# Optimization experiments

Hardware: AMD Instinct MI355X
Metric: run time of the kernel (lower is better)

## Reference

```python
import jax, jax.numpy as jnp
import numpy as np

B, TQ, TK, D, H = 8, 1024, 1024, 1024, 16
HD = D // H
EPS = 1e-5


def layernorm(x, g, b):
    mu = jnp.mean(x, axis=-1, keepdims=True)
    var = jnp.mean(jnp.square(x - mu), axis=-1, keepdims=True)
    return (x - mu) * jax.lax.rsqrt(var + EPS) * g + b


def setup_inputs() -> dict:
    key = jax.random.key(0)
    ks = jax.random.split(key, 16)
    s = 1.0 / np.sqrt(D)
    return {
        "base": jax.random.normal(ks[0], (B, TQ, D), jnp.float32),
        "fusion": jax.random.normal(ks[1], (B, TK, D), jnp.float32),
        "Wq": jax.random.normal(ks[2], (D, D), jnp.float32) * s,
        "Wk": jax.random.normal(ks[3], (D, D), jnp.float32) * s,
        "Wv": jax.random.normal(ks[4], (D, D), jnp.float32) * s,
        "Wo": jax.random.normal(ks[5], (D, D), jnp.float32) * s,
        "g1": jnp.ones((D,), jnp.float32),
        "b1": jnp.zeros((D,), jnp.float32),
        "g2": jnp.ones((D,), jnp.float32),
        "b2": jnp.zeros((D,), jnp.float32),
        "fc1_w": jax.random.normal(ks[6], (D, D), jnp.float32) * s,
        "fc1_b": jnp.zeros((D,), jnp.float32),
        "fc2_w": jax.random.normal(ks[7], (D, D), jnp.float32) * s,
        "fc2_b": jnp.zeros((D,), jnp.float32),
        "rw": jax.random.normal(ks[8], (D, D), jnp.float32) * s,
        "rb": jnp.zeros((D,), jnp.float32),
        "alpha": jnp.asarray(0.1, jnp.float32),
    }


def reference(base, fusion, Wq, Wk, Wv, Wo, g1, b1, g2, b2,
              fc1_w, fc1_b, fc2_w, fc2_b, rw, rb, alpha):
    def split_heads(x):  # [B,T,D] -> [B,H,T,hd]
        return x.reshape(B, -1, H, HD).transpose(0, 2, 1, 3)

    Q = split_heads(base @ Wq.T)
    K = split_heads(fusion @ Wk.T)
    V = split_heads(fusion @ Wv.T)

    scores = jnp.einsum("bhqd,bhkd->bhqk", Q, K) / jnp.sqrt(jnp.float32(HD))
    attn = jax.nn.softmax(scores, axis=-1)
    # threshold mask (the torch scatter_ with arange indices is an identity copy)
    masked = attn * (attn >= alpha).astype(attn.dtype)
    # second softmax over masked weights (zeros contribute exp(0)=1, as in the original)
    attn2 = jax.nn.softmax(masked, axis=-1)
    out = jnp.einsum("bhqk,bhkd->bhqd", attn2, V)
    out = out.transpose(0, 2, 1, 3).reshape(B, TQ, D)
    out = out @ Wo.T
    x = layernorm(base + out, g1, b1)  # dropout is eval-mode identity
    ff = jax.nn.silu(jax.nn.silu(x @ fc1_w.T + fc1_b) @ fc2_w.T + fc2_b)
    y = layernorm(x + ff, g2, b2)
    final = y @ rw.T + rb
    return final, masked
```

## Files before the change

kernel.cpp:

```cpp
#include <hip/hip_runtime.h>


typedef unsigned short u16;
typedef __attribute__((ext_vector_type(8))) short  bf16x8;
typedef __attribute__((ext_vector_type(4))) float  f32x4;

#define GLL16(gp, lp) __builtin_amdgcn_global_load_lds(                     \
    (__attribute__((address_space(1))) const void*)(gp),                    \
    (__attribute__((address_space(3))) void*)(lp), 16, 0, 0)

__device__ __forceinline__ u16 f2bf(float x) {
  union { float f; unsigned u; } v; v.f = x;
  return (u16)((v.u + 0x7FFF + ((v.u >> 16) & 1)) >> 16);
}
__device__ __forceinline__ f32x4 zero4() { f32x4 z = {0.f, 0.f, 0.f, 0.f}; return z; }

__global__ __launch_bounds__(256) void pack_act(const float* __restrict__ a,
                                                const float* __restrict__ b,
                                                u16* __restrict__ outa,
                                                u16* __restrict__ outb) {
  size_t i = (size_t)blockIdx.x * 256 + threadIdx.x;
  const float* in = blockIdx.y ? b : a;
  u16* out = blockIdx.y ? outb : outa;
  out[i] = f2bf(in[i]);
}

__global__ __launch_bounds__(256) void pack_w(
    const float* __restrict__ w0, const float* __restrict__ w1,
    const float* __restrict__ w2, const float* __restrict__ w3,
    const float* __restrict__ w4, const float* __restrict__ w5,
    const float* __restrict__ w6, u16* __restrict__ out) {
  size_t i = (size_t)blockIdx.x * 256 + threadIdx.x;
  const float* in;
  switch (blockIdx.y) {
    case 0: in = w0; break;  case 1: in = w1; break;
    case 2: in = w2; break;  case 3: in = w3; break;
    case 4: in = w4; break;  case 5: in = w5; break;
    default: in = w6; break;
  }
  out[(size_t)blockIdx.y * 1048576 + i] = f2bf(in[i]);
}

#define EPI_QKV       0
#define EPI_F32       3
#define EPI_SILU_BF16 4
#define EPI_SILU_F32  5
#define EPI_BIAS_F32  6

template <int EPI>
__global__ __launch_bounds__(256) void gemm_bt(
    const u16* __restrict__ A, int lda,
    const u16* __restrict__ W, int ldw,
    int M, int N, int K,
    float* __restrict__ outF, u16* __restrict__ outU,
    const float* __restrict__ bias,
    const u16* __restrict__ A2) {
  __shared__ u16 As[128 * 32];
  __shared__ u16 Bs[128 * 32];
  int tid = threadIdx.x;
  int l = tid & 63, w = tid >> 6;
  int wr = w >> 1, wc = w & 1, lr = l & 15, lq = l >> 4;
  int m0 = blockIdx.y * 128, n0 = blockIdx.x * 128;

  const u16* Ap = A;
  const u16* Wp = W;
  u16* outUp = outU;
  if constexpr (EPI == EPI_QKV) {
    int z = blockIdx.z;
    if (z) Ap = A2;
    Wp = W + (size_t)z * 1048576;
    outUp = outU + (size_t)z * 8388608;
  }

  f32x4 acc[4][4];
#pragma unroll
  for (int i = 0; i < 4; i++)
#pragma unroll
    for (int j = 0; j < 4; j++) acc[i][j] = zero4();

  auto stage = [&](const u16* src, int ld, int r0, int k0, u16* lds) {
#pragma unroll
    for (int j = 0; j < 2; ++j) {
      int seg = j * 256 + tid;
      int row = seg >> 2, sp = seg & 3;
      const u16* g = src + (size_t)(r0 + row) * ld + k0 +
                     ((sp ^ ((row >> 1) & 3)) << 3);
      GLL16(g, lds + seg * 8);
    }
  };

  int nk = K >> 5;
  stage(Ap, lda, m0, 0, As);
  stage(Wp, ldw, n0, 0, Bs);
  for (int kt = 0; kt < nk; ++kt) {
    __syncthreads();
    bf16x8 af[4], bw[4];
    int slot = (lq ^ ((lr >> 1) & 3)) << 3;
#pragma unroll
    for (int mi = 0; mi < 4; mi++)
      af[mi] = *(const bf16x8*)&As[(wr * 64 + mi * 16 + lr) * 32 + slot];
#pragma unroll
    for (int ni = 0; ni < 4; ni++)
      bw[ni] = *(const bf16x8*)&Bs[(wc * 64 + ni * 16 + lr) * 32 + slot];
#pragma unroll
    for (int mi = 0; mi < 4; mi++)
#pragma unroll
      for (int ni = 0; ni < 4; ni++)
        acc[mi][ni] = __builtin_amdgcn_mfma_f32_16x16x32_bf16(af[mi], bw[ni],
                                                              acc[mi][ni], 0, 0, 0);
    __syncthreads();
    if (kt + 1 < nk) {
      stage(Ap, lda, m0, (kt + 1) << 5, As);
      stage(Wp, ldw, n0, (kt + 1) << 5, Bs);
    }
  }

#pragma unroll
  for (int mi = 0; mi < 4; mi++) {
#pragma unroll
    for (int ni = 0; ni < 4; ni++) {
      int col = n0 + wc * 64 + ni * 16 + lr;
#pragma unroll
      for (int r = 0; r < 4; r++) {
        int row = m0 + wr * 64 + mi * 16 + lq * 4 + r;
        float v = acc[mi][ni][r];
        if constexpr (EPI == EPI_QKV) {
          int b = row >> 10, t = row & 1023, h = col >> 6, d = col & 63;
          int z = blockIdx.z;
          if (z == 0) {
            outUp[((size_t)(b * 16 + h) * 1024 + t) * 64 + d] = f2bf(v);
          } else if (z == 1) {
            size_t base = ((size_t)(b * 16 + h) * 1024 + t) * 64;
            outUp[base + (((d >> 3) ^ (t & 7)) << 3) + (d & 7)] = f2bf(v);
          } else {
            size_t o = ((size_t)(b * 16 + h) * 64 + d) * 1024 + (t & ~63) +
                       ((((t >> 3) & 7) ^ (d & 7)) << 3) + (t & 7);
            outUp[o] = f2bf(v);
          }
        } else if constexpr (EPI == EPI_F32) {
          outF[(size_t)row * N + col] = v;
        } else if constexpr (EPI == EPI_SILU_BF16) {
          float z = v + bias[col];
          outUp[(size_t)row * N + col] = f2bf(z / (1.f + __expf(-z)));
        } else if constexpr (EPI == EPI_SILU_F32) {
          float z = v + bias[col];
          outF[(size_t)row * N + col] = z / (1.f + __expf(-z));
        } else {
          outF[(size_t)row * N + col] = v + bias[col];
        }
      }
    }
  }
}

__global__ __launch_bounds__(256) void attn_kernel(
    const u16* __restrict__ Q2, const u16* __restrict__ K2,
    const u16* __restrict__ Vt, const float* __restrict__ alphap,
    float* __restrict__ masked_out, u16* __restrict__ attn_out) {
  __shared__ __align__(16) u16 Ks[64 * 64];
  __shared__ __align__(16) u16 Vs[64 * 64];
  __shared__ __align__(16) u16 Ps[4][2][16 * 72];

  int tid = threadIdx.x;
  int l = tid & 63, w = tid >> 6, lr = l & 15, lq = l >> 4;
  int q0 = blockIdx.x * 128;
  int h = blockIdx.y, b = blockIdx.z;
  int bh = b * 16 + h;
  const u16* Qb = Q2 + (size_t)bh * 1024 * 64;
  const u16* Kb = K2 + (size_t)bh * 1024 * 64;
  const u16* Vb = Vt + (size_t)bh * 64 * 1024;
  float alpha = alphap[0];
  int qw = q0 + w * 32;

  bf16x8 qf[2][2];
#pragma unroll
  for (int s = 0; s < 2; s++)
#pragma unroll
    for (int kt = 0; kt < 2; kt++)
      qf[s][kt] = *(const bf16x8*)(Qb + (size_t)(qw + s * 16 + lr) * 64 + kt * 32 + lq * 8);

  float s1[2][4] = {{0.f, 0.f, 0.f, 0.f}, {0.f, 0.f, 0.f, 0.f}};

  for (int kc = 0; kc < 16; ++kc) {
    __syncthreads();
#pragma unroll
    for (int j = 0; j < 2; ++j) {
      int seg = j * 256 + tid;
      GLL16(Kb + (size_t)kc * 4096 + seg * 8, Ks + seg * 8);
    }
    __syncthreads();
    f32x4 acc[2][4];
#pragma unroll
    for (int s = 0; s < 2; s++)
#pragma unroll
      for (int ni = 0; ni < 4; ni++) acc[s][ni] = zero4();
#pragma unroll
    for (int ni = 0; ni < 4; ++ni) {
      int t = ni * 16 + lr;
      bf16x8 k0 = *(const bf16x8*)&Ks[t * 64 + (((0 + lq) ^ (lr & 7)) << 3)];
      bf16x8 k1 = *(const bf16x8*)&Ks[t * 64 + (((4 + lq) ^ (lr & 7)) << 3)];
#pragma unroll
      for (int s = 0; s < 2; s++) {
        acc[s][ni] = __builtin_amdgcn_mfma_f32_16x16x32_bf16(qf[s][0], k0, acc[s][ni], 0, 0, 0);
        acc[s][ni] = __builtin_amdgcn_mfma_f32_16x16x32_bf16(qf[s][1], k1, acc[s][ni], 0, 0, 0);
      }
    }
#pragma unroll
    for (int s = 0; s < 2; s++)
#pragma unroll
      for (int ni = 0; ni < 4; ni++)
#pragma unroll
        for (int r = 0; r < 4; r++)
          s1[s][r] += __expf(acc[s][ni][r] * 0.125f);
  }
#pragma unroll
  for (int s = 0; s < 2; s++)
#pragma unroll
    for (int r = 0; r < 4; r++) {
      float v = s1[s][r];
      v += __shfl_xor(v, 1); v += __shfl_xor(v, 2);
      v += __shfl_xor(v, 4); v += __shfl_xor(v, 8);
      s1[s][r] = 1.0f / v;
    }

  float s2[2][4] = {{0.f, 0.f, 0.f, 0.f}, {0.f, 0.f, 0.f, 0.f}};
  f32x4 oacc[2][4];
#pragma unroll
  for (int s = 0; s < 2; s++)
#pragma unroll
    for (int dg = 0; dg < 4; dg++) oacc[s][dg] = zero4();

  for (int kc = 0; kc < 16; ++kc) {
    __syncthreads();
#pragma unroll
    for (int j = 0; j < 2; ++j) {
      int seg = j * 256 + tid;
      GLL16(Kb + (size_t)kc * 4096 + seg * 8, Ks + seg * 8);
    }
#pragma unroll
    for (int j = 0; j < 2; ++j) {
      int seg = j * 256 + tid;
      GLL16(Vb + (size_t)(seg >> 3) * 1024 + kc * 64 + (seg & 7) * 8, Vs + seg * 8);
    }
    __syncthreads();

    f32x4 acc[2][4];
#pragma unroll
    for (int s = 0; s < 2; s++)
#pragma unroll
      for (int ni = 0; ni < 4; ni++) acc[s][ni] = zero4();
#pragma unroll
    for (int ni = 0; ni < 4; ++ni) {
      int t = ni * 16 + lr;
      bf16x8 k0 = *(const bf16x8*)&Ks[t * 64 + (((0 + lq) ^ (lr & 7)) << 3)];
      bf16x8 k1 = *(const bf16x8*)&Ks[t * 64 + (((4 + lq) ^ (lr & 7)) << 3)];
#pragma unroll
      for (int s = 0; s < 2; s++) {
        acc[s][ni] = __builtin_amdgcn_mfma_f32_16x16x32_bf16(qf[s][0], k0, acc[s][ni], 0, 0, 0);
        acc[s][ni] = __builtin_amdgcn_mfma_f32_16x16x32_bf16(qf[s][1], k1, acc[s][ni], 0, 0, 0);
      }
    }

#pragma unroll
    for (int s = 0; s < 2; s++) {
#pragma unroll
      for (int ni = 0; ni < 4; ni++) {
#pragma unroll
        for (int r = 0; r < 4; r++) {
          float e = __expf(acc[s][ni][r] * 0.125f);
          float a = e * s1[s][r];
          a = (a >= alpha) ? a : 0.0f;
          size_t row = (size_t)bh * 1024 + qw + s * 16 + lq * 4 + r;
          masked_out[row * 1024 + kc * 64 + ni * 16 + lr] = a;
          float p = __expf(a);
          s2[s][r] += p;
          Ps[w][s][(lq * 4 + r) * 72 + ni * 16 + lr] = f2bf(p);
        }
      }
    }
    __syncthreads();

    bf16x8 pf[2][2];
#pragma unroll
    for (int s = 0; s < 2; s++)
#pragma unroll
      for (int kt = 0; kt < 2; kt++)
        pf[s][kt] = *(const bf16x8*)&Ps[w][s][lr * 72 + kt * 32 + lq * 8];
#pragma unroll
    for (int dg = 0; dg < 4; dg++) {
      int d = dg * 16 + lr;
      bf16x8 v0 = *(const bf16x8*)&Vs[d * 64 + (((0 + lq) ^ (lr & 7)) << 3)];
      bf16x8 v1 = *(const bf16x8*)&Vs[d * 64 + (((4 + lq) ^ (lr & 7)) << 3)];
#pragma unroll
      for (int s = 0; s < 2; s++) {
        oacc[s][dg] = __builtin_amdgcn_mfma_f32_16x16x32_bf16(pf[s][0], v0, oacc[s][dg], 0, 0, 0);
        oacc[s][dg] = __builtin_amdgcn_mfma_f32_16x16x32_bf16(pf[s][1], v1, oacc[s][dg], 0, 0, 0);
      }
    }
  }

#pragma unroll
  for (int s = 0; s < 2; s++)
#pragma unroll
    for (int r = 0; r < 4; r++) {
      float v = s2[s][r];
      v += __shfl_xor(v, 1); v += __shfl_xor(v, 2);
      v += __shfl_xor(v, 4); v += __shfl_xor(v, 8);
      s2[s][r] = 1.0f / v;
    }
#pragma unroll
  for (int s = 0; s < 2; s++)
#pragma unroll
    for (int dg = 0; dg < 4; dg++)
#pragma unroll
      for (int r = 0; r < 4; r++) {
        int q = qw + s * 16 + lq * 4 + r;
        attn_out[(size_t)(b * 1024 + q) * 1024 + h * 64 + dg * 16 + lr] =
            f2bf(oacc[s][dg][r] * s2[s][r]);
      }
}

__global__ __launch_bounds__(256) void ln_kernel(
    const float* __restrict__ A, const float* __restrict__ Bv,
    const float* __restrict__ g, const float* __restrict__ beta,
    float* __restrict__ outF, u16* __restrict__ outB) {
  __shared__ float red[4];
  int row = blockIdx.x, t = threadIdx.x;
  const float* pa = A + (size_t)row * 1024;
  const float* pb = Bv + (size_t)row * 1024;
  float v[4];
  float s = 0.f;
#pragma unroll
  for (int i = 0; i < 4; i++) { int c = t + 256 * i; v[i] = pa[c] + pb[c]; s += v[i]; }
#pragma unroll
  for (int off = 1; off < 64; off <<= 1) s += __shfl_xor(s, off);
  if ((t & 63) == 0) red[t >> 6] = s;
  __syncthreads();
  s = red[0] + red[1] + red[2] + red[3];
  float mu = s * 0.0009765625f;
  float q = 0.f;
#pragma unroll
  for (int i = 0; i < 4; i++) { float d = v[i] - mu; q += d * d; }
  __syncthreads();
#pragma unroll
  for (int off = 1; off < 64; off <<= 1) q += __shfl_xor(q, off);
  if ((t & 63) == 0) red[t >> 6] = q;
  __syncthreads();
  q = red[0] + red[1] + red[2] + red[3];
  float rs = rsqrtf(q * 0.0009765625f + 1e-5f);
#pragma unroll
  for (int i = 0; i < 4; i++) {
    int c = t + 256 * i;
    float y = (v[i] - mu) * rs * g[c] + beta[c];
    if (outF) outF[(size_t)row * 1024 + c] = y;
    if (outB) outB[(size_t)row * 1024 + c] = f2bf(y);
  }
}

#define WS_BASEB   0
#define WS_FUSB    16777216
#define WS_W       33554432
#define WS_QKV     48234496
#define WS_ATTNO   98566144
#define WS_O       115343360
#define WS_X       148897792
#define WS_XB      WS_BASEB
#define WS_H1      WS_ATTNO
#define WS_FF      WS_QKV
#define WS_YB      (WS_QKV + 33554432)

extern "C" void kernel_launch(void* const* d_in, const int* in_sizes, int n_in,
                              void* d_out, int out_size, void* d_ws, size_t ws_size,
                              hipStream_t stream) {
  const float* base   = (const float*)d_in[0];
  const float* fusion = (const float*)d_in[1];
  const float* Wq     = (const float*)d_in[2];
  const float* Wk     = (const float*)d_in[3];
  const float* Wv     = (const float*)d_in[4];
  const float* Wo     = (const float*)d_in[5];
  const float* g1     = (const float*)d_in[6];
  const float* b1     = (const float*)d_in[7];
  const float* g2     = (const float*)d_in[8];
  const float* b2     = (const float*)d_in[9];
  const float* fc1w   = (const float*)d_in[10];
  const float* fc1b   = (const float*)d_in[11];
  const float* fc2w   = (const float*)d_in[12];
  const float* fc2b   = (const float*)d_in[13];
  const float* rw     = (const float*)d_in[14];
  const float* rb     = (const float*)d_in[15];
  const float* alphap = (const float*)d_in[16];

  char* ws = (char*)d_ws;
  u16* baseb  = (u16*)(ws + WS_BASEB);
  u16* fusb   = (u16*)(ws + WS_FUSB);
  u16* wall   = (u16*)(ws + WS_W);
  u16* Q2     = (u16*)(ws + WS_QKV);
  u16* attno  = (u16*)(ws + WS_ATTNO);
  float* obuf = (float*)(ws + WS_O);
  float* x    = (float*)(ws + WS_X);
  u16* xb     = (u16*)(ws + WS_XB);
  u16* h1     = (u16*)(ws + WS_H1);
  float* ff   = (float*)(ws + WS_FF);
  u16* yb     = (u16*)(ws + WS_YB);

  float* final_out  = (float*)d_out;
  float* masked_out = final_out + 8388608;

  pack_act<<<dim3(32768, 2), 256, 0, stream>>>(base, fusion, baseb, fusb);
  pack_w<<<dim3(4096, 7), 256, 0, stream>>>(Wq, Wk, Wv, Wo, fc1w, fc2w, rw, wall);

  dim3 gg(8, 64);

  gemm_bt<EPI_QKV><<<dim3(8, 64, 3), 256, 0, stream>>>(
      baseb, 1024, wall, 1024, 8192, 1024, 1024, nullptr, Q2, nullptr, fusb);

  attn_kernel<<<dim3(8, 16, 8), 256, 0, stream>>>(
      Q2, Q2 + 8388608, Q2 + 16777216, alphap, masked_out, attno);

  gemm_bt<EPI_F32><<<gg, 256, 0, stream>>>(attno, 1024, wall + 3 * 1048576, 1024,
                                           8192, 1024, 1024, obuf, nullptr, nullptr, nullptr);
  ln_kernel<<<8192, 256, 0, stream>>>(base, obuf, g1, b1, x, xb);

  gemm_bt<EPI_SILU_BF16><<<gg, 256, 0, stream>>>(xb, 1024, wall + 4 * 1048576, 1024,
                                                 8192, 1024, 1024, nullptr, h1, fc1b, nullptr);
  gemm_bt<EPI_SILU_F32><<<gg, 256, 0, stream>>>(h1, 1024, wall + 5 * 1048576, 1024,
                                                8192, 1024, 1024, ff, nullptr, fc2b, nullptr);
  ln_kernel<<<8192, 256, 0, stream>>>(x, ff, g2, b2, nullptr, yb);

  gemm_bt<EPI_BIAS_F32><<<gg, 256, 0, stream>>>(yb, 1024, wall + 6 * 1048576, 1024,
                                                8192, 1024, 1024, final_out, nullptr, rb, nullptr);
}
```

Baseline: 1.054 ms.

## Double-buffer LDS tiles in GEMM and attention; store intermediates as bf16

The GEMM and both attention passes now use ping-pong LDS buffers. The next K/V or A/W tile is issued with global_load_lds before the current tile is computed, which removes one barrier per iteration. The Wo and fc2 GEMM outputs are written as bf16 instead of fp32, and the layernorm kernel reads them as bf16, halving intermediate traffic at some precision cost. In the attention PV stage a barrier is replaced by an lgkmcnt wait. With one barrier per iteration, the async global-to-LDS loads into the other buffer may not be fenced correctly, which risks a race.

```diff
diff --git a/kernel.cpp b/kernel.cpp
--- a/kernel.cpp
+++ b/kernel.cpp
@@ -12,6 +12,10 @@
 __device__ __forceinline__ u16 f2bf(float x) {
   union { float f; unsigned u; } v; v.f = x;
   return (u16)((v.u + 0x7FFF + ((v.u >> 16) & 1)) >> 16);
+}
+__device__ __forceinline__ float bf2f(u16 h) {
+  union { unsigned u; float f; } v; v.u = ((unsigned)h) << 16;
+  return v.f;
 }
 __device__ __forceinline__ f32x4 zero4() { f32x4 z = {0.f, 0.f, 0.f, 0.f}; return z; }
 
@@ -42,9 +46,8 @@
 }
 
 #define EPI_QKV       0
-#define EPI_F32       3
+#define EPI_BF16      1
 #define EPI_SILU_BF16 4
-#define EPI_SILU_F32  5
 #define EPI_BIAS_F32  6
 
 template <int EPI>
@@ -55,8 +58,8 @@
     float* __restrict__ outF, u16* __restrict__ outU,
     const float* __restrict__ bias,
     const u16* __restrict__ A2) {
-  __shared__ u16 As[128 * 32];
-  __shared__ u16 Bs[128 * 32];
+  __shared__ u16 As[2][128 * 32];
+  __shared__ u16 Bs[2][128 * 32];
   int tid = threadIdx.x;
   int l = tid & 63, w = tid >> 6;
   int wr = w >> 1, wc = w & 1, lr = l & 15, lq = l >> 4;
@@ -90,29 +93,30 @@
   };
 
   int nk = K >> 5;
-  stage(Ap, lda, m0, 0, As);
-  stage(Wp, ldw, n0, 0, Bs);
+  stage(Ap, lda, m0, 0, As[0]);
+  stage(Wp, ldw, n0, 0, Bs[0]);
   for (int kt = 0; kt < nk; ++kt) {
     __syncthreads();
+    if (kt + 1 < nk) {
+      stage(Ap, lda, m0, (kt + 1) << 5, As[(kt + 1) & 1]);
+      stage(Wp, ldw, n0, (kt + 1) << 5, Bs[(kt + 1) & 1]);
+    }
+    const u16* Ab = As[kt & 1];
+    const u16* Bb = Bs[kt & 1];
     bf16x8 af[4], bw[4];
     int slot = (lq ^ ((lr >> 1) & 3)) << 3;
 #pragma unroll
     for (int mi = 0; mi < 4; mi++)
-      af[mi] = *(const bf16x8*)&As[(wr * 64 + mi * 16 + lr) * 32 + slot];
+      af[mi] = *(const bf16x8*)&Ab[(wr * 64 + mi * 16 + lr) * 32 + slot];
 #pragma unroll
     for (int ni = 0; ni < 4; ni++)
-      bw[ni] = *(const bf16x8*)&Bs[(wc * 64 + ni * 16 + lr) * 32 + slot];
+      bw[ni] = *(const bf16x8*)&Bb[(wc * 64 + ni * 16 + lr) * 32 + slot];
 #pragma unroll
     for (int mi = 0; mi < 4; mi++)
 #pragma unroll
       for (int ni = 0; ni < 4; ni++)
         acc[mi][ni] = __builtin_amdgcn_mfma_f32_16x16x32_bf16(af[mi], bw[ni],
                                                               acc[mi][ni], 0, 0, 0);
-    __syncthreads();
-    if (kt + 1 < nk) {
-      stage(Ap, lda, m0, (kt + 1) << 5, As);
-      stage(Wp, ldw, n0, (kt + 1) << 5, Bs);
-    }
   }
 
 #pragma unroll
@@ -137,14 +141,11 @@
                        ((((t >> 3) & 7) ^ (d & 7)) << 3) + (t & 7);
             outUp[o] = f2bf(v);
           }
-        } else if constexpr (EPI == EPI_F32) {
-          outF[(size_t)row * N + col] = v;
+        } else if constexpr (EPI == EPI_BF16) {
+          outUp[(size_t)row * N + col] = f2bf(v);
         } else if constexpr (EPI == EPI_SILU_BF16) {
           float z = v + bias[col];
           outUp[(size_t)row * N + col] = f2bf(z / (1.f + __expf(-z)));
-        } else if constexpr (EPI == EPI_SILU_F32) {
-          float z = v + bias[col];
-          outF[(size_t)row * N + col] = z / (1.f + __expf(-z));
         } else {
           outF[(size_t)row * N + col] = v + bias[col];
         }
@@ -157,8 +158,8 @@
     const u16* __restrict__ Q2, const u16* __restrict__ K2,
     const u16* __restrict__ Vt, const float* __restrict__ alphap,
     float* __restrict__ masked_out, u16* __restrict__ attn_out) {
-  __shared__ __align__(16) u16 Ks[64 * 64];
-  __shared__ __align__(16) u16 Vs[64 * 64];
+  __shared__ __align__(16) u16 Ks[2][4096];
+  __shared__ __align__(16) u16 Vs[2][4096];
   __shared__ __align__(16) u16 Ps[4][2][16 * 72];
 
   int tid = threadIdx.x;
@@ -172,6 +173,21 @@
   float alpha = alphap[0];
   int qw = q0 + w * 32;
 
+  auto stageK = [&](int kc, u16* dst) {
+#pragma unroll
+    for (int j = 0; j < 2; ++j) {
+      int seg = j * 256 + tid;
+      GLL16(Kb + (size_t)kc * 4096 + seg * 8, dst + seg * 8);
+    }
+  };
+  auto stageV = [&](int kc, u16* dst) {
+#pragma unroll
+    for (int j = 0; j < 2; ++j) {
+      int seg = j * 256 + tid;
+      GLL16(Vb + (size_t)(seg >> 3) * 1024 + kc * 64 + (seg & 7) * 8, dst + seg * 8);
+    }
+  };
+
   bf16x8 qf[2][2];
 #pragma unroll
   for (int s = 0; s < 2; s++)
@@ -181,14 +197,11 @@
 
   float s1[2][4] = {{0.f, 0.f, 0.f, 0.f}, {0.f, 0.f, 0.f, 0.f}};
 
+  stageK(0, Ks[0]);
   for (int kc = 0; kc < 16; ++kc) {
     __syncthreads();
-#pragma unroll
-    for (int j = 0; j < 2; ++j) {
-      int seg = j * 256 + tid;
-      GLL16(Kb + (size_t)kc * 4096 + seg * 8, Ks + seg * 8);
-    }
-    __syncthreads();
+    if (kc + 1 < 16) stageK(kc + 1, Ks[(kc + 1) & 1]);
+    const u16* Kc = Ks[kc & 1];
     f32x4 acc[2][4];
 #pragma unroll
     for (int s = 0; s < 2; s++)
@@ -197,8 +210,8 @@
 #pragma unroll
     for (int ni = 0; ni < 4; ++ni) {
       int t = ni * 16 + lr;
-      bf16x8 k0 = *(const bf16x8*)&Ks[t * 64 + (((0 + lq) ^ (lr & 7)) << 3)];
-      bf16x8 k1 = *(const bf16x8*)&Ks[t * 64 + (((4 + lq) ^ (lr & 7)) << 3)];
+      bf16x8 k0 = *(const bf16x8*)&Kc[t * 64 + (((0 + lq) ^ (lr & 7)) << 3)];
+      bf16x8 k1 = *(const bf16x8*)&Kc[t * 64 + (((4 + lq) ^ (lr & 7)) << 3)];
 #pragma unroll
       for (int s = 0; s < 2; s++) {
         acc[s][ni] = __builtin_amdgcn_mfma_f32_16x16x32_bf16(qf[s][0], k0, acc[s][ni], 0, 0, 0);
@@ -230,19 +243,16 @@
 #pragma unroll
     for (int dg = 0; dg < 4; dg++) oacc[s][dg] = zero4();
 
+  stageK(0, Ks[0]);
+  stageV(0, Vs[0]);
   for (int kc = 0; kc < 16; ++kc) {
     __syncthreads();
-#pragma unroll
-    for (int j = 0; j < 2; ++j) {
-      int seg = j * 256 + tid;
-      GLL16(Kb + (size_t)kc * 4096 + seg * 8, Ks + seg * 8);
-    }
-#pragma unroll
-    for (int j = 0; j < 2; ++j) {
-      int seg = j * 256 + tid;
-      GLL16(Vb + (size_t)(seg >> 3) * 1024 + kc * 64 + (seg & 7) * 8, Vs + seg * 8);
-    }
-    __syncthreads();
+    if (kc + 1 < 16) {
+      stageK(kc + 1, Ks[(kc + 1) & 1]);
+      stageV(kc + 1, Vs[(kc + 1) & 1]);
+    }
+    const u16* Kc = Ks[kc & 1];
+    const u16* Vc = Vs[kc & 1];
 
     f32x4 acc[2][4];
 #pragma unroll
@@ -252,8 +262,8 @@
 #pragma unroll
     for (int ni = 0; ni < 4; ++ni) {
       int t = ni * 16 + lr;
-      bf16x8 k0 = *(const bf16x8*)&Ks[t * 64 + (((0 + lq) ^ (lr & 7)) << 3)];
-      bf16x8 k1 = *(const bf16x8*)&Ks[t * 64 + (((4 + lq) ^ (lr & 7)) << 3)];
+      bf16x8 k0 = *(const bf16x8*)&Kc[t * 64 + (((0 + lq) ^ (lr & 7)) << 3)];
+      bf16x8 k1 = *(const bf16x8*)&Kc[t * 64 + (((4 + lq) ^ (lr & 7)) << 3)];
 #pragma unroll
       for (int s = 0; s < 2; s++) {
         acc[s][ni] = __builtin_amdgcn_mfma_f32_16x16x32_bf16(qf[s][0], k0, acc[s][ni], 0, 0, 0);
@@ -278,7 +288,7 @@
         }
       }
     }
-    __syncthreads();
+    asm volatile("s_waitcnt lgkmcnt(0)" ::: "memory");
 
     bf16x8 pf[2][2];
 #pragma unroll
@@ -289,8 +299,8 @@
 #pragma unroll
     for (int dg = 0; dg < 4; dg++) {
       int d = dg * 16 + lr;
-      bf16x8 v0 = *(const bf16x8*)&Vs[d * 64 + (((0 + lq) ^ (lr & 7)) << 3)];
-      bf16x8 v1 = *(const bf16x8*)&Vs[d * 64 + (((4 + lq) ^ (lr & 7)) << 3)];
+      bf16x8 v0 = *(const bf16x8*)&Vc[d * 64 + (((0 + lq) ^ (lr & 7)) << 3)];
+      bf16x8 v1 = *(const bf16x8*)&Vc[d * 64 + (((4 + lq) ^ (lr & 7)) << 3)];
 #pragma unroll
       for (int s = 0; s < 2; s++) {
         oacc[s][dg] = __builtin_amdgcn_mfma_f32_16x16x32_bf16(pf[s][0], v0, oacc[s][dg], 0, 0, 0);
@@ -321,17 +331,21 @@
 }
 
 __global__ __launch_bounds__(256) void ln_kernel(
-    const float* __restrict__ A, const float* __restrict__ Bv,
+    const float* __restrict__ A, const u16* __restrict__ Bv,
     const float* __restrict__ g, const float* __restrict__ beta,
     float* __restrict__ outF, u16* __restrict__ outB) {
   __shared__ float red[4];
   int row = blockIdx.x, t = threadIdx.x;
   const float* pa = A + (size_t)row * 1024;
-  const float* pb = Bv + (size_t)row * 1024;
+  const u16* pb = Bv + (size_t)row * 1024;
   float v[4];
   float s = 0.f;
 #pragma unroll
-  for (int i = 0; i < 4; i++) { int c = t + 256 * i; v[i] = pa[c] + pb[c]; s += v[i]; }
+  for (int i = 0; i < 4; i++) {
+    int c = t + 256 * i;
+    v[i] = pa[c] + bf2f(pb[c]);
+    s += v[i];
+  }
 #pragma unroll
   for (int off = 1; off < 64; off <<= 1) s += __shfl_xor(s, off);
   if ((t & 63) == 0) red[t >> 6] = s;
@@ -362,12 +376,12 @@
 #define WS_W       33554432
 #define WS_QKV     48234496
 #define WS_ATTNO   98566144
-#define WS_O       115343360
-#define WS_X       148897792
+#define WS_X       115343360
+#define WS_OB      WS_FUSB
 #define WS_XB      WS_BASEB
 #define WS_H1      WS_ATTNO
-#define WS_FF      WS_QKV
-#define WS_YB      (WS_QKV + 33554432)
+#define WS_FFB     WS_QKV
+#define WS_YB      (WS_QKV + 16777216)
 
 extern "C" void kernel_launch(void* const* d_in, const int* in_sizes, int n_in,
                               void* d_out, int out_size, void* d_ws, size_t ws_size,
@@ -396,11 +410,11 @@
   u16* wall   = (u16*)(ws + WS_W);
   u16* Q2     = (u16*)(ws + WS_QKV);
   u16* attno  = (u16*)(ws + WS_ATTNO);
-  float* obuf = (float*)(ws + WS_O);
+  u16* obufb  = (u16*)(ws + WS_OB);
   float* x    = (float*)(ws + WS_X);
   u16* xb     = (u16*)(ws + WS_XB);
   u16* h1     = (u16*)(ws + WS_H1);
-  float* ff   = (float*)(ws + WS_FF);
+  u16* ffb    = (u16*)(ws + WS_FFB);
   u16* yb     = (u16*)(ws + WS_YB);
 
   float* final_out  = (float*)d_out;
@@ -417,15 +431,15 @@
   attn_kernel<<<dim3(8, 16, 8), 256, 0, stream>>>(
       Q2, Q2 + 8388608, Q2 + 16777216, alphap, masked_out, attno);
 
-  gemm_bt<EPI_F32><<<gg, 256, 0, stream>>>(attno, 1024, wall + 3 * 1048576, 1024,
-                                           8192, 1024, 1024, obuf, nullptr, nullptr, nullptr);
-  ln_kernel<<<8192, 256, 0, stream>>>(base, obuf, g1, b1, x, xb);
+  gemm_bt<EPI_BF16><<<gg, 256, 0, stream>>>(attno, 1024, wall + 3 * 1048576, 1024,
+                                            8192, 1024, 1024, nullptr, obufb, nullptr, nullptr);
+  ln_kernel<<<8192, 256, 0, stream>>>(base, obufb, g1, b1, x, xb);
 
   gemm_bt<EPI_SILU_BF16><<<gg, 256, 0, stream>>>(xb, 1024, wall + 4 * 1048576, 1024,
                                                  8192, 1024, 1024, nullptr, h1, fc1b, nullptr);
-  gemm_bt<EPI_SILU_F32><<<gg, 256, 0, stream>>>(h1, 1024, wall + 5 * 1048576, 1024,
-                                                8192, 1024, 1024, ff, nullptr, fc2b, nullptr);
-  ln_kernel<<<8192, 256, 0, stream>>>(x, ff, g2, b2, nullptr, yb);
+  gemm_bt<EPI_SILU_BF16><<<gg, 256, 0, stream>>>(h1, 1024, wall + 5 * 1048576, 1024,
+                                                 8192, 1024, 1024, nullptr, ffb, fc2b, nullptr);
+  ln_kernel<<<8192, 256, 0, stream>>>(x, ffb, g2, b2, nullptr, yb);
 
   gemm_bt<EPI_BIAS_F32><<<gg, 256, 0, stream>>>(yb, 1024, wall + 6 * 1048576, 1024,
                                                 8192, 1024, 1024, final_out, nullptr, rb, nullptr);
```

Measured after the change: 1.014 ms. -3.8%, faster.
